# Kernel tuning notes

Measured on AMD Instinct MI355X. Metric: run time of the kernel, lower is better.

Reference implementation:

```python
import jax, jax.numpy as jnp
import numpy as np

HEADS = 12
DIM_HEAD = 64
SCALE = DIM_HEAD ** -0.5


def setup_inputs() -> dict:
    key = jax.random.key(0)
    ks = jax.random.split(key, 7)
    b, n, dim = 16, 1024, 768
    inner = HEADS * DIM_HEAD
    x = jax.random.normal(ks[0], (b, n, dim), dtype=jnp.float32)
    Wq = jax.random.normal(ks[1], (dim, inner), dtype=jnp.float32) * (dim ** -0.5)
    Wkv = jax.random.normal(ks[2], (dim, 2 * inner), dtype=jnp.float32) * (dim ** -0.5)
    mix_pre = jax.random.normal(ks[3], (HEADS, HEADS), dtype=jnp.float32)
    mix_post = jax.random.normal(ks[4], (HEADS, HEADS), dtype=jnp.float32)
    Wo = jax.random.normal(ks[5], (inner, dim), dtype=jnp.float32) * (inner ** -0.5)
    bo = jnp.zeros((dim,), dtype=jnp.float32)
    return {"x": x, "Wq": Wq, "Wkv": Wkv, "mix_pre": mix_pre,
            "mix_post": mix_post, "Wo": Wo, "bo": bo}


def reference(x, Wq, Wkv, mix_pre, mix_post, Wo, bo):
    b, n, dim = x.shape
    h, d = HEADS, DIM_HEAD
    # projections (context is None -> context = x)
    q = (x @ Wq).reshape(b, n, h, d).transpose(0, 2, 1, 3)        # b h n d
    kv = x @ Wkv
    k = kv[..., : h * d].reshape(b, n, h, d).transpose(0, 2, 1, 3)
    v = kv[..., h * d:].reshape(b, n, h, d).transpose(0, 2, 1, 3)
    # scaled QK^T
    attn = jnp.einsum('bhid,bhjd->bhij', q, k) * SCALE             # b h n n
    # talking-heads pre-softmax: mix over head dim
    attn = jnp.einsum('bhij,hg->bgij', attn, mix_pre)
    attn = jax.nn.softmax(attn, axis=-1)
    # talking-heads post-softmax
    attn = jnp.einsum('bhij,hg->bgij', attn, mix_post)
    out = jnp.einsum('bhij,bhjd->bhid', attn, v)                   # b h n d
    out = out.transpose(0, 2, 1, 3).reshape(b, n, h * d)           # b n (h d)
    return out @ Wo + bo
```

## Files before the change

kernel.cpp:

```cpp
#include <hip/hip_runtime.h>


typedef _Float16 f16;
typedef _Float16 f16x8 __attribute__((ext_vector_type(8)));
typedef _Float16 f16x4 __attribute__((ext_vector_type(4)));
typedef float f32x4 __attribute__((ext_vector_type(4)));
typedef float fv4 __attribute__((ext_vector_type(4)));

#define MFMA(a, b, c) __builtin_amdgcn_mfma_f32_16x16x32_f16(a, b, c, 0, 0, 0)
#define MFMA16(a, b, c) __builtin_amdgcn_mfma_f32_16x16x16f16(a, b, c, 0, 0, 0)

__global__ __launch_bounds__(256) void k_cast_x(const float* __restrict__ x,
                                                f16* __restrict__ xb) {
  int idx = (blockIdx.x * 256 + threadIdx.x) * 8;
  fv4 a = *(const fv4*)(x + idx);
  fv4 b = *(const fv4*)(x + idx + 4);
  f16x8 o;
  o[0] = (f16)a[0]; o[1] = (f16)a[1]; o[2] = (f16)a[2]; o[3] = (f16)a[3];
  o[4] = (f16)b[0]; o[5] = (f16)b[1]; o[6] = (f16)b[2]; o[7] = (f16)b[3];
  *(f16x8*)(xb + idx) = o;
}

__global__ __launch_bounds__(256) void k_prep_w(const float* __restrict__ Wq,
                                                const float* __restrict__ Wkv,
                                                const float* __restrict__ Wo,
                                                f16* __restrict__ Wt,
                                                f16* __restrict__ WoT) {
  int idx = blockIdx.x * 256 + threadIdx.x;
  if (idx < 2304 * 768) {
    int n = idx / 768, k = idx % 768;
    float v = (n < 768) ? Wq[k * 768 + n] * 0.125f
                        : Wkv[k * 1536 + (n - 768)];
    Wt[idx] = (f16)v;
  } else {
    int id2 = idx - 2304 * 768;
    int n = id2 / 768, k = id2 % 768;
    WoT[id2] = (f16)Wo[k * 768 + n];
  }
}

__global__ __launch_bounds__(256) void k_gemm_qkv(const f16* __restrict__ A,
                                                  const f16* __restrict__ Bt,
                                                  f16* __restrict__ qb,
                                                  f16* __restrict__ kb,
                                                  f16* __restrict__ vb) {
  __shared__ f16 As[128 * 72];
  __shared__ f16 Bs[128 * 72];
  const int tid = threadIdx.x;
  const int m0 = blockIdx.y << 7;
  const int n0 = blockIdx.x << 7;
  const int lane = tid & 63, w = tid >> 6;
  const int quad = lane >> 4, col = lane & 15;
  const int wm = (w >> 1) << 6, wn = (w & 1) << 6;
  const f32x4 z4 = {0.f, 0.f, 0.f, 0.f};
  f32x4 acc[4][4];
#pragma unroll
  for (int i = 0; i < 4; ++i)
#pragma unroll
    for (int j = 0; j < 4; ++j) acc[i][j] = z4;

  for (int k0 = 0; k0 < 768; k0 += 64) {
#pragma unroll
    for (int s = 0; s < 4; ++s) {
      int u = s * 256 + tid;
      int row = u >> 3, seg = (u & 7) << 3;
      *(f16x8*)&As[row * 72 + seg] = *(const f16x8*)(A + (m0 + row) * 768 + k0 + seg);
      *(f16x8*)&Bs[row * 72 + seg] = *(const f16x8*)(Bt + (n0 + row) * 768 + k0 + seg);
    }
    __syncthreads();
#pragma unroll
    for (int kk = 0; kk < 64; kk += 32) {
      f16x8 af[4], bf[4];
#pragma unroll
      for (int ic = 0; ic < 4; ++ic)
        af[ic] = *(f16x8*)&As[(wm + ic * 16 + col) * 72 + kk + quad * 8];
#pragma unroll
      for (int jc = 0; jc < 4; ++jc)
        bf[jc] = *(f16x8*)&Bs[(wn + jc * 16 + col) * 72 + kk + quad * 8];
#pragma unroll
      for (int ic = 0; ic < 4; ++ic)
#pragma unroll
        for (int jc = 0; jc < 4; ++jc) acc[ic][jc] = MFMA(af[ic], bf[jc], acc[ic][jc]);
    }
    __syncthreads();
  }
#pragma unroll
  for (int jc = 0; jc < 4; ++jc) {
    int gn = n0 + wn + jc * 16 + col;
#pragma unroll
    for (int ic = 0; ic < 4; ++ic)
#pragma unroll
      for (int r = 0; r < 4; ++r) {
        int gm = m0 + wm + ic * 16 + (quad << 2) + r;
        int b = gm >> 10, i = gm & 1023;
        f16 v = (f16)acc[ic][jc][r];
        if (gn < 768) {
          int h = gn >> 6, dd = gn & 63;
          qb[(((b * 12 + h) << 10) + i) * 64 + dd] = v;
        } else if (gn < 1536) {
          int t = gn - 768; int h = t >> 6, dd = t & 63;
          kb[(((b * 12 + h) << 10) + i) * 64 + dd] = v;
        } else {
          int t = gn - 1536; int h = t >> 6, dd = t & 63;
          vb[(((b * 12 + h) << 10) + i) * 64 + dd] = v;
        }
      }
  }
}

__global__ __launch_bounds__(256) void k_transpose_v(const f16* __restrict__ vb,
                                                     f16* __restrict__ vt) {
  __shared__ f16 t[64 * 72];
  const int bh = blockIdx.x;
  const int n0 = blockIdx.y << 6;
  const int tid = threadIdx.x;
#pragma unroll
  for (int s = 0; s < 2; ++s) {
    int u = s * 256 + tid;
    int r = u >> 3, c = (u & 7) << 3;
    *(f16x8*)&t[r * 72 + c] = *(const f16x8*)(vb + (bh * 1024 + n0 + r) * 64 + c);
  }
  __syncthreads();
#pragma unroll
  for (int s = 0; s < 2; ++s) {
    int u = s * 256 + tid;
    int d = u >> 3, c = (u & 7) << 3;
    f16x8 o;
#pragma unroll
    for (int e = 0; e < 8; ++e) o[e] = t[(c + e) * 72 + d];
    *(f16x8*)(vt + (bh * 64 + d) * 1024 + n0 + c) = o;
  }
}

__global__ __launch_bounds__(256, 2) void k_attn(
    const f16* __restrict__ qb, const f16* __restrict__ kb, const f16* __restrict__ vt,
    const float* __restrict__ mixp, const float* __restrict__ mixq,
    f16* __restrict__ ob) {
  __shared__ f16 Slds[4][4096];
  __shared__ f16 Pmb[12 * 16 * 16 * 4];

  const int tid = threadIdx.x;
  const int bid0 = blockIdx.x;
  const int bid = ((bid0 & 7) << 7) | (bid0 >> 3);
  const int b = bid >> 6;
  const int i0 = (bid & 63) << 4;
  const int lane = tid & 63;
  const int w = tid >> 6;
  const int quad = lane >> 4, col = lane & 15;
  const int q4 = quad << 2;
  const int w3 = w * 3;
  const int jw = w << 4;
  const f32x4 z4 = {0.f, 0.f, 0.f, 0.f};

  f16x4 b_pre, b_post;
#pragma unroll
  for (int e = 0; e < 4; ++e) {
    int hk = q4 + e;
    bool ok = (hk < 12) && (col < 12);
    b_pre[e]  = ok ? (f16)mixp[hk * 12 + col] : (f16)0.f;
    b_post[e] = ok ? (f16)mixq[hk * 12 + col] : (f16)0.f;
  }

  f16* Sw = &Slds[w][0];
  {
    f16x4 z; z[0] = (f16)0.f; z[1] = (f16)0.f; z[2] = (f16)0.f; z[3] = (f16)0.f;
#pragma unroll
    for (int u = 0; u < 4; ++u) {
      int idx = u * 64 + lane;
      *(f16x4*)&Sw[(((idx >> 4) << 6) + 48 + (idx & 15)) * 4] = z;
    }
  }

  f16x8 qf[12][2];
#pragma unroll
  for (int h = 0; h < 12; ++h)
#pragma unroll
    for (int kc = 0; kc < 2; ++kc)
      qf[h][kc] = *(const f16x8*)(qb + ((((b * 12 + h) << 10) + i0 + col) << 6) +
                                  kc * 32 + quad * 8);

  auto stage = [&](int j0) {
#pragma unroll
    for (int hg = 0; hg < 3; ++hg) {
      f32x4 s4[4];
#pragma unroll
      for (int e = 0; e < 4; ++e) {
        int h = hg * 4 + e;
        const f16* kbase = kb + ((((b * 12 + h) << 10) + j0 + jw + col) << 6);
        f16x8 kf0 = *(const f16x8*)(kbase + quad * 8);
        f16x8 kf1 = *(const f16x8*)(kbase + 32 + quad * 8);
        f32x4 a = MFMA(qf[h][0], kf0, z4);
        s4[e] = MFMA(qf[h][1], kf1, a);
      }
#pragma unroll
      for (int r = 0; r < 4; ++r) {
        f16x4 p;
        p[0] = (f16)s4[0][r]; p[1] = (f16)s4[1][r];
        p[2] = (f16)s4[2][r]; p[3] = (f16)s4[3][r];
        *(f16x4*)&Sw[((col << 6) + hg * 16 + ((q4 + r + col) & 15)) * 4] = p;
      }
    }
  };

  float l_run[4] = {0.f, 0.f, 0.f, 0.f};
  for (int j0 = 0; j0 < 1024; j0 += 64) {
    stage(j0);
#pragma unroll
    for (int t = 0; t < 16; ++t) {
      f16x4 sB = *(const f16x4*)&Sw[((t << 6) + quad * 16 + ((col + t) & 15)) * 4];
      f32x4 d1 = MFMA16(b_pre, sB, z4);
#pragma unroll
      for (int r = 0; r < 4; ++r) l_run[r] += __expf(d1[r]);
    }
  }
  float* Lb = (float*)Pmb;
#pragma unroll
  for (int r = 0; r < 4; ++r) Lb[(w * 16 + q4 + r) * 16 + col] = l_run[r];
  __syncthreads();
  float il[4];
#pragma unroll
  for (int r = 0; r < 4; ++r) {
    float s = 0.f;
#pragma unroll
    for (int ww = 0; ww < 4; ++ww) s += Lb[(ww * 16 + q4 + r) * 16 + col];
    il[r] = 1.f / s;
  }
  __syncthreads();

  f32x4 oa[3][4];
#pragma unroll
  for (int g = 0; g < 3; ++g)
#pragma unroll
    for (int dc = 0; dc < 4; ++dc) oa[g][dc] = z4;

  for (int j0 = 0; j0 < 1024; j0 += 64) {
    stage(j0);
#pragma unroll
    for (int tt = 0; tt < 4; ++tt) {
      f16x4 pk[4];
#pragma unroll
      for (int t4 = 0; t4 < 4; ++t4) {
        int t = tt * 4 + t4;
        f16x4 sB = *(const f16x4*)&Sw[((t << 6) + quad * 16 + ((col + t) & 15)) * 4];
        f32x4 d1 = MFMA16(b_pre, sB, z4);
        f16x4 pA;
#pragma unroll
        for (int r = 0; r < 4; ++r) pA[r] = (f16)(__expf(d1[r]) * il[r]);
        f32x4 d2 = MFMA16(pA, b_post, z4);
#pragma unroll
        for (int r = 0; r < 4; ++r) pk[r][t4] = (f16)d2[r];
      }
      if (col < 12) {
#pragma unroll
        for (int r = 0; r < 4; ++r) {
          int k4 = (col + q4 + r) & 15;
          *(f16x4*)&Pmb[(((col << 4) + q4 + r) * 16 + ((w * 4 + tt) ^ k4)) * 4] = pk[r];
        }
      }
    }
    __syncthreads();
    __builtin_amdgcn_s_setprio(1);
#pragma unroll
    for (int gg = 0; gg < 3; ++gg) {
      int gp = w3 + gg;
      int k4r = (gp + col) & 15;
#pragma unroll
      for (int jh = 0; jh < 2; ++jh) {
        int ub = (jh * 4 + quad) * 2;
        f16x4 lo = *(const f16x4*)&Pmb[(((gp << 4) + col) * 16 + (ub ^ k4r)) * 4];
        f16x4 hi = *(const f16x4*)&Pmb[(((gp << 4) + col) * 16 + ((ub + 1) ^ k4r)) * 4];
        f16x8 aP = __builtin_shufflevector(lo, hi, 0, 1, 2, 3, 4, 5, 6, 7);
#pragma unroll
        for (int dc = 0; dc < 4; ++dc) {
          f16x8 vf = *(const f16x8*)(vt + ((((b * 12 + gp) << 6) + dc * 16 + col) << 10) +
                                     j0 + jh * 32 + quad * 8);
          oa[gg][dc] = MFMA(aP, vf, oa[gg][dc]);
        }
      }
    }
    __builtin_amdgcn_s_setprio(0);
    __syncthreads();
  }

#pragma unroll
  for (int gg = 0; gg < 3; ++gg) {
    int gp = w3 + gg;
#pragma unroll
    for (int dc = 0; dc < 4; ++dc)
#pragma unroll
      for (int r = 0; r < 4; ++r)
        ob[((b << 10) + i0 + q4 + r) * 768 + gp * 64 + dc * 16 + col] =
            (f16)oa[gg][dc][r];
  }
}

__global__ __launch_bounds__(256) void k_gemm_out(const f16* __restrict__ A,
                                                  const f16* __restrict__ Bt,
                                                  const float* __restrict__ bias,
                                                  float* __restrict__ out) {
  __shared__ f16 As[128 * 72];
  __shared__ f16 Bs[128 * 72];
  const int tid = threadIdx.x;
  const int m0 = blockIdx.y << 7;
  const int n0 = blockIdx.x << 7;
  const int lane = tid & 63, w = tid >> 6;
  const int quad = lane >> 4, col = lane & 15;
  const int wm = (w >> 1) << 6, wn = (w & 1) << 6;
  const f32x4 z4 = {0.f, 0.f, 0.f, 0.f};
  f32x4 acc[4][4];
#pragma unroll
  for (int i = 0; i < 4; ++i)
#pragma unroll
    for (int j = 0; j < 4; ++j) acc[i][j] = z4;

  for (int k0 = 0; k0 < 768; k0 += 64) {
#pragma unroll
    for (int s = 0; s < 4; ++s) {
      int u = s * 256 + tid;
      int row = u >> 3, seg = (u & 7) << 3;
      *(f16x8*)&As[row * 72 + seg] = *(const f16x8*)(A + (m0 + row) * 768 + k0 + seg);
      *(f16x8*)&Bs[row * 72 + seg] = *(const f16x8*)(Bt + (n0 + row) * 768 + k0 + seg);
    }
    __syncthreads();
#pragma unroll
    for (int kk = 0; kk < 64; kk += 32) {
      f16x8 af[4], bf[4];
#pragma unroll
      for (int ic = 0; ic < 4; ++ic)
        af[ic] = *(f16x8*)&As[(wm + ic * 16 + col) * 72 + kk + quad * 8];
#pragma unroll
      for (int jc = 0; jc < 4; ++jc)
        bf[jc] = *(f16x8*)&Bs[(wn + jc * 16 + col) * 72 + kk + quad * 8];
#pragma unroll
      for (int ic = 0; ic < 4; ++ic)
#pragma unroll
        for (int jc = 0; jc < 4; ++jc) acc[ic][jc] = MFMA(af[ic], bf[jc], acc[ic][jc]);
    }
    __syncthreads();
  }
#pragma unroll
  for (int jc = 0; jc < 4; ++jc) {
    int gn = n0 + wn + jc * 16 + col;
    float bv = bias[gn];
#pragma unroll
    for (int ic = 0; ic < 4; ++ic)
#pragma unroll
      for (int r = 0; r < 4; ++r) {
        int gm = m0 + wm + ic * 16 + (quad << 2) + r;
        out[gm * 768 + gn] = acc[ic][jc][r] + bv;
      }
  }
}

extern "C" void kernel_launch(void* const* d_in, const int* in_sizes, int n_in,
                              void* d_out, int out_size, void* d_ws, size_t ws_size,
                              hipStream_t stream) {
  const float* x    = (const float*)d_in[0];
  const float* Wq   = (const float*)d_in[1];
  const float* Wkv  = (const float*)d_in[2];
  const float* mixp = (const float*)d_in[3];
  const float* mixq = (const float*)d_in[4];
  const float* Wo   = (const float*)d_in[5];
  const float* bo   = (const float*)d_in[6];
  float* out = (float*)d_out;

  char* ws = (char*)d_ws;
  f16* xb  = (f16*)(ws);
  f16* Wt  = (f16*)(ws + 25165824);
  f16* WoT = (f16*)(ws + 28704768);
  f16* qb  = (f16*)(ws + 29884416);
  f16* kb  = (f16*)(ws + 55050240);
  f16* vb  = (f16*)(ws + 80216064);
  f16* vt  = xb;
  f16* obuf = vb;

  k_cast_x<<<dim3(6144), dim3(256), 0, stream>>>(x, xb);
  k_prep_w<<<dim3(9216), dim3(256), 0, stream>>>(Wq, Wkv, Wo, Wt, WoT);
  k_gemm_qkv<<<dim3(18, 128), dim3(256), 0, stream>>>(xb, Wt, qb, kb, vb);
  k_transpose_v<<<dim3(192, 16), dim3(256), 0, stream>>>(vb, vt);
  k_attn<<<dim3(1024), dim3(256), 0, stream>>>(qb, kb, vt, mixp, mixq, obuf);
  k_gemm_out<<<dim3(6, 128), dim3(256), 0, stream>>>(obuf, WoT, bo, out);
}
```

Baseline: 827.8 us.

## Process 32 query rows per attention block with 8 waves

Each attention block now covers 32 query rows with 512 threads (8 waves) instead of 16 rows with 4 waves. Two wave groups split the rows and share the P-matrix exchange, so each block's V loads serve twice as many query rows. Shared memory becomes dynamic and grows to 112 KB per block, which limits how many blocks fit per CU and can lower occupancy.

```diff
diff --git a/kernel.cpp b/kernel.cpp
--- a/kernel.cpp
+++ b/kernel.cpp
@@ -132,24 +132,26 @@
   }
 }
 
-__global__ __launch_bounds__(256, 2) void k_attn(
+__global__ __launch_bounds__(512, 2) void k_attn(
     const f16* __restrict__ qb, const f16* __restrict__ kb, const f16* __restrict__ vt,
     const float* __restrict__ mixp, const float* __restrict__ mixq,
     f16* __restrict__ ob) {
-  __shared__ f16 Slds[4][4096];
-  __shared__ f16 Pmb[12 * 16 * 16 * 4];
+  extern __shared__ f16 smem[];
+  f16* Slds = smem;
+  f16* Pmb  = smem + 8 * 4096;
 
   const int tid = threadIdx.x;
   const int bid0 = blockIdx.x;
-  const int bid = ((bid0 & 7) << 7) | (bid0 >> 3);
-  const int b = bid >> 6;
-  const int i0 = (bid & 63) << 4;
+  const int bid = ((bid0 & 7) << 6) | (bid0 >> 3);
+  const int b = bid >> 5;
+  const int i0 = (bid & 31) << 5;
   const int lane = tid & 63;
   const int w = tid >> 6;
   const int quad = lane >> 4, col = lane & 15;
   const int q4 = quad << 2;
-  const int w3 = w * 3;
-  const int jw = w << 4;
+  const int ih = w >> 2;
+  const int jq = w & 3;
+  const int jw = jq << 4;
   const f32x4 z4 = {0.f, 0.f, 0.f, 0.f};
 
   f16x4 b_pre, b_post;
@@ -161,7 +163,7 @@
     b_post[e] = ok ? (f16)mixq[hk * 12 + col] : (f16)0.f;
   }
 
-  f16* Sw = &Slds[w][0];
+  f16* Sw = &Slds[w * 4096];
   {
     f16x4 z; z[0] = (f16)0.f; z[1] = (f16)0.f; z[2] = (f16)0.f; z[3] = (f16)0.f;
 #pragma unroll
@@ -176,7 +178,7 @@
   for (int h = 0; h < 12; ++h)
 #pragma unroll
     for (int kc = 0; kc < 2; ++kc)
-      qf[h][kc] = *(const f16x8*)(qb + ((((b * 12 + h) << 10) + i0 + col) << 6) +
+      qf[h][kc] = *(const f16x8*)(qb + ((((b * 12 + h) << 10) + i0 + ih * 16 + col) << 6) +
                                   kc * 32 + quad * 8);
 
   auto stage = [&](int j0) {
@@ -215,14 +217,14 @@
   }
   float* Lb = (float*)Pmb;
 #pragma unroll
-  for (int r = 0; r < 4; ++r) Lb[(w * 16 + q4 + r) * 16 + col] = l_run[r];
+  for (int r = 0; r < 4; ++r) Lb[w * 256 + (q4 + r) * 16 + col] = l_run[r];
   __syncthreads();
   float il[4];
 #pragma unroll
   for (int r = 0; r < 4; ++r) {
     float s = 0.f;
 #pragma unroll
-    for (int ww = 0; ww < 4; ++ww) s += Lb[(ww * 16 + q4 + r) * 16 + col];
+    for (int jj = 0; jj < 4; ++jj) s += Lb[(ih * 4 + jj) * 256 + (q4 + r) * 16 + col];
     il[r] = 1.f / s;
   }
   __syncthreads();
@@ -253,8 +255,9 @@
       if (col < 12) {
 #pragma unroll
         for (int r = 0; r < 4; ++r) {
-          int k4 = (col + q4 + r) & 15;
-          *(f16x4*)&Pmb[(((col << 4) + q4 + r) * 16 + ((w * 4 + tt) ^ k4)) * 4] = pk[r];
+          int iL = ih * 16 + q4 + r;
+          int k4 = (col + iL) & 15;
+          *(f16x4*)&Pmb[((col * 32 + iL) * 16 + (((jq << 2) + tt) ^ k4)) * 4] = pk[r];
         }
       }
     }
@@ -262,13 +265,15 @@
     __builtin_amdgcn_s_setprio(1);
 #pragma unroll
     for (int gg = 0; gg < 3; ++gg) {
-      int gp = w3 + gg;
-      int k4r = (gp + col) & 15;
+      int id = w * 3 + gg;
+      int gp = id >> 1, ihp = id & 1;
+      int row = gp * 32 + ihp * 16 + col;
+      int k4r = (gp + ihp * 16 + col) & 15;
 #pragma unroll
       for (int jh = 0; jh < 2; ++jh) {
         int ub = (jh * 4 + quad) * 2;
-        f16x4 lo = *(const f16x4*)&Pmb[(((gp << 4) + col) * 16 + (ub ^ k4r)) * 4];
-        f16x4 hi = *(const f16x4*)&Pmb[(((gp << 4) + col) * 16 + ((ub + 1) ^ k4r)) * 4];
+        f16x4 lo = *(const f16x4*)&Pmb[(row * 16 + (ub ^ k4r)) * 4];
+        f16x4 hi = *(const f16x4*)&Pmb[(row * 16 + ((ub + 1) ^ k4r)) * 4];
         f16x8 aP = __builtin_shufflevector(lo, hi, 0, 1, 2, 3, 4, 5, 6, 7);
 #pragma unroll
         for (int dc = 0; dc < 4; ++dc) {
@@ -284,12 +289,13 @@
 
 #pragma unroll
   for (int gg = 0; gg < 3; ++gg) {
-    int gp = w3 + gg;
+    int id = w * 3 + gg;
+    int gp = id >> 1, ihp = id & 1;
 #pragma unroll
     for (int dc = 0; dc < 4; ++dc)
 #pragma unroll
       for (int r = 0; r < 4; ++r)
-        ob[((b << 10) + i0 + q4 + r) * 768 + gp * 64 + dc * 16 + col] =
+        ob[((b << 10) + i0 + ihp * 16 + q4 + r) * 768 + gp * 64 + dc * 16 + col] =
             (f16)oa[gg][dc][r];
   }
 }
@@ -378,6 +384,6 @@
   k_prep_w<<<dim3(9216), dim3(256), 0, stream>>>(Wq, Wkv, Wo, Wt, WoT);
   k_gemm_qkv<<<dim3(18, 128), dim3(256), 0, stream>>>(xb, Wt, qb, kb, vb);
   k_transpose_v<<<dim3(192, 16), dim3(256), 0, stream>>>(vb, vt);
-  k_attn<<<dim3(1024), dim3(256), 0, stream>>>(qb, kb, vt, mixp, mixq, obuf);
+  k_attn<<<dim3(512), dim3(512), 114688, stream>>>(qb, kb, vt, mixp, mixq, obuf);
   k_gemm_out<<<dim3(6, 128), dim3(256), 0, stream>>>(obuf, WoT, bo, out);
 }
```

Measured after the change: 872.7 us. 1.05x slower.

## Stage Q tile in swizzled LDS instead of registers and compact score buffer

Applied to the files above, without the earlier changes.

The per-thread Q fragments (24 f16x8 registers) are moved into a swizzled shared-memory tile that is reloaded inside each QK^T stage, with the aim of cutting VGPR pressure in the attention kernel. The per-wave score buffer is compacted from 4096 to 3200 halves, so the unused fourth head group now reads a single shared zero row. Shared memory moves to a dynamic allocation of about 73 KB per block. In exchange, every stage issues extra LDS reads, and the larger LDS footprint may itself cap occupancy below the two blocks per CU the launch bounds target.

```diff
diff --git a/kernel.cpp b/kernel.cpp
--- a/kernel.cpp
+++ b/kernel.cpp
@@ -136,8 +136,10 @@
     const f16* __restrict__ qb, const f16* __restrict__ kb, const f16* __restrict__ vt,
     const float* __restrict__ mixp, const float* __restrict__ mixq,
     f16* __restrict__ ob) {
-  __shared__ f16 Slds[4][4096];
-  __shared__ f16 Pmb[12 * 16 * 16 * 4];
+  extern __shared__ f16 smem[];
+  f16* Qs   = smem;
+  f16* Slds = smem + 12288;
+  f16* Pmb  = smem + 25088;
 
   const int tid = threadIdx.x;
   const int bid0 = blockIdx.x;
@@ -161,23 +163,20 @@
     b_post[e] = ok ? (f16)mixq[hk * 12 + col] : (f16)0.f;
   }
 
-  f16* Sw = &Slds[w][0];
-  {
+  f16* Sw = &Slds[w * 3200];
+  if (lane < 16) {
     f16x4 z; z[0] = (f16)0.f; z[1] = (f16)0.f; z[2] = (f16)0.f; z[3] = (f16)0.f;
-#pragma unroll
-    for (int u = 0; u < 4; ++u) {
-      int idx = u * 64 + lane;
-      *(f16x4*)&Sw[(((idx >> 4) << 6) + 48 + (idx & 15)) * 4] = z;
-    }
-  }
-
-  f16x8 qf[12][2];
-#pragma unroll
-  for (int h = 0; h < 12; ++h)
-#pragma unroll
-    for (int kc = 0; kc < 2; ++kc)
-      qf[h][kc] = *(const f16x8*)(qb + ((((b * 12 + h) << 10) + i0 + col) << 6) +
-                                  kc * 32 + quad * 8);
+    *(f16x4*)&Sw[3072 + lane * 4] = z;
+  }
+
+#pragma unroll
+  for (int s = 0; s < 6; ++s) {
+    int u = s * 256 + tid;
+    int h = u >> 7, i = (u >> 3) & 15, uu = u & 7;
+    f16x8 q = *(const f16x8*)(qb + ((((b * 12 + h) << 10) + i0 + i) << 6) + uu * 8);
+    *(f16x8*)&Qs[(((h << 4) + i) << 6) + ((uu ^ (i & 7)) << 3)] = q;
+  }
+  __syncthreads();
 
   auto stage = [&](int j0) {
 #pragma unroll
@@ -189,17 +188,26 @@
         const f16* kbase = kb + ((((b * 12 + h) << 10) + j0 + jw + col) << 6);
         f16x8 kf0 = *(const f16x8*)(kbase + quad * 8);
         f16x8 kf1 = *(const f16x8*)(kbase + 32 + quad * 8);
-        f32x4 a = MFMA(qf[h][0], kf0, z4);
-        s4[e] = MFMA(qf[h][1], kf1, a);
+        f16x8 q0 = *(const f16x8*)&Qs[(((h << 4) + col) << 6) +
+                                      ((quad ^ (col & 7)) << 3)];
+        f16x8 q1 = *(const f16x8*)&Qs[(((h << 4) + col) << 6) +
+                                      (((4 + quad) ^ (col & 7)) << 3)];
+        f32x4 a = MFMA(q0, kf0, z4);
+        s4[e] = MFMA(q1, kf1, a);
       }
 #pragma unroll
       for (int r = 0; r < 4; ++r) {
         f16x4 p;
         p[0] = (f16)s4[0][r]; p[1] = (f16)s4[1][r];
         p[2] = (f16)s4[2][r]; p[3] = (f16)s4[3][r];
-        *(f16x4*)&Sw[((col << 6) + hg * 16 + ((q4 + r + col) & 15)) * 4] = p;
-      }
-    }
+        *(f16x4*)&Sw[col * 192 + hg * 64 + ((q4 + r + col) & 15) * 4] = p;
+      }
+    }
+  };
+  auto sread = [&](int t) -> f16x4 {
+    int zi = (quad < 3) ? (t * 192 + quad * 64 + ((col + t) & 15) * 4)
+                        : (3072 + ((col + t) & 15) * 4);
+    return *(const f16x4*)&Sw[zi];
   };
 
   float l_run[4] = {0.f, 0.f, 0.f, 0.f};
@@ -207,7 +215,7 @@
     stage(j0);
 #pragma unroll
     for (int t = 0; t < 16; ++t) {
-      f16x4 sB = *(const f16x4*)&Sw[((t << 6) + quad * 16 + ((col + t) & 15)) * 4];
+      f16x4 sB = sread(t);
       f32x4 d1 = MFMA16(b_pre, sB, z4);
 #pragma unroll
       for (int r = 0; r < 4; ++r) l_run[r] += __expf(d1[r]);
@@ -241,7 +249,7 @@
 #pragma unroll
       for (int t4 = 0; t4 < 4; ++t4) {
         int t = tt * 4 + t4;
-        f16x4 sB = *(const f16x4*)&Sw[((t << 6) + quad * 16 + ((col + t) & 15)) * 4];
+        f16x4 sB = sread(t);
         f32x4 d1 = MFMA16(b_pre, sB, z4);
         f16x4 pA;
 #pragma unroll
@@ -378,6 +386,6 @@
   k_prep_w<<<dim3(9216), dim3(256), 0, stream>>>(Wq, Wkv, Wo, Wt, WoT);
   k_gemm_qkv<<<dim3(18, 128), dim3(256), 0, stream>>>(xb, Wt, qb, kb, vb);
   k_transpose_v<<<dim3(192, 16), dim3(256), 0, stream>>>(vb, vt);
-  k_attn<<<dim3(1024), dim3(256), 0, stream>>>(qb, kb, vt, mixp, mixq, obuf);
+  k_attn<<<dim3(1024), dim3(256), 74752, stream>>>(qb, kb, vt, mixp, mixq, obuf);
   k_gemm_out<<<dim3(6, 128), dim3(256), 0, stream>>>(obuf, WoT, bo, out);
 }
```

New measurement: 770.3 us. -6.9%, faster.

## Restructure attention kernel to 8 waves with head/column split and double-buffered LDS

Applied to the files above, without the earlier changes.

The attention kernel now runs 8 waves per block instead of 4. Each wave owns 3 heads and one 16-column half of a 32-wide key chunk, replacing the 12-head-per-wave staging, so each wave holds fewer Q fragments in registers. S and P tiles are double-buffered in dynamic shared memory, V fragments are prefetched before the barrier, and blocks are remapped so each XCD handles whole batches. The aim is to cut register pressure and raise occupancy and latency hiding, at the cost of extra block-wide syncs per chunk and more LDS per block.

```diff
diff --git a/kernel.cpp b/kernel.cpp
--- a/kernel.cpp
+++ b/kernel.cpp
@@ -132,88 +132,85 @@
   }
 }
 
-__global__ __launch_bounds__(256, 2) void k_attn(
+__global__ __launch_bounds__(512, 4) void k_attn(
     const f16* __restrict__ qb, const f16* __restrict__ kb, const f16* __restrict__ vt,
     const float* __restrict__ mixp, const float* __restrict__ mixq,
     f16* __restrict__ ob) {
-  __shared__ f16 Slds[4][4096];
-  __shared__ f16 Pmb[12 * 16 * 16 * 4];
+  extern __shared__ f16 smem[];
 
   const int tid = threadIdx.x;
   const int bid0 = blockIdx.x;
-  const int bid = ((bid0 & 7) << 7) | (bid0 >> 3);
-  const int b = bid >> 6;
-  const int i0 = (bid & 63) << 4;
+  const int xcd = bid0 & 7, idx = bid0 >> 3;
+  const int b = ((idx >> 6) << 3) | xcd;
+  const int i0 = (idx & 63) << 4;
   const int lane = tid & 63;
   const int w = tid >> 6;
   const int quad = lane >> 4, col = lane & 15;
   const int q4 = quad << 2;
-  const int w3 = w * 3;
-  const int jw = w << 4;
+  const int hh = w >> 1;
+  const int jh = w & 1;
   const f32x4 z4 = {0.f, 0.f, 0.f, 0.f};
 
   f16x4 b_pre, b_post;
 #pragma unroll
   for (int e = 0; e < 4; ++e) {
+    b_pre[e]  = (e < 3 && col < 12) ? (f16)mixp[(3 * quad + e) * 12 + col] : (f16)0.f;
     int hk = q4 + e;
-    bool ok = (hk < 12) && (col < 12);
-    b_pre[e]  = ok ? (f16)mixp[hk * 12 + col] : (f16)0.f;
-    b_post[e] = ok ? (f16)mixq[hk * 12 + col] : (f16)0.f;
-  }
-
-  f16* Sw = &Slds[w][0];
-  {
-    f16x4 z; z[0] = (f16)0.f; z[1] = (f16)0.f; z[2] = (f16)0.f; z[3] = (f16)0.f;
-#pragma unroll
-    for (int u = 0; u < 4; ++u) {
-      int idx = u * 64 + lane;
-      *(f16x4*)&Sw[(((idx >> 4) << 6) + 48 + (idx & 15)) * 4] = z;
-    }
-  }
-
-  f16x8 qf[12][2];
-#pragma unroll
-  for (int h = 0; h < 12; ++h)
+    b_post[e] = (hk < 12 && col < 12) ? (f16)mixq[hk * 12 + col] : (f16)0.f;
+  }
+
+  f16x8 qf[3][2];
+#pragma unroll
+  for (int e = 0; e < 3; ++e)
 #pragma unroll
     for (int kc = 0; kc < 2; ++kc)
-      qf[h][kc] = *(const f16x8*)(qb + ((((b * 12 + h) << 10) + i0 + col) << 6) +
+      qf[e][kc] = *(const f16x8*)(qb + ((((b * 12 + 3 * hh + e) << 10) + i0 + col) << 6) +
                                   kc * 32 + quad * 8);
 
-  auto stage = [&](int j0) {
-#pragma unroll
-    for (int hg = 0; hg < 3; ++hg) {
-      f32x4 s4[4];
-#pragma unroll
-      for (int e = 0; e < 4; ++e) {
-        int h = hg * 4 + e;
-        const f16* kbase = kb + ((((b * 12 + h) << 10) + j0 + jw + col) << 6);
-        f16x8 kf0 = *(const f16x8*)(kbase + quad * 8);
-        f16x8 kf1 = *(const f16x8*)(kbase + 32 + quad * 8);
-        f32x4 a = MFMA(qf[h][0], kf0, z4);
-        s4[e] = MFMA(qf[h][1], kf1, a);
-      }
-#pragma unroll
-      for (int r = 0; r < 4; ++r) {
-        f16x4 p;
-        p[0] = (f16)s4[0][r]; p[1] = (f16)s4[1][r];
-        p[2] = (f16)s4[2][r]; p[3] = (f16)s4[3][r];
-        *(f16x4*)&Sw[((col << 6) + hg * 16 + ((q4 + r + col) & 15)) * 4] = p;
-      }
+  auto computeS = [&](int j0, f16* Sw) {
+    f16x8 kr[3][2];
+#pragma unroll
+    for (int e = 0; e < 3; ++e) {
+      const f16* kbase =
+          kb + ((((b * 12 + 3 * hh + e) << 10) + j0 + jh * 16 + col) << 6);
+      kr[e][0] = *(const f16x8*)(kbase + quad * 8);
+      kr[e][1] = *(const f16x8*)(kbase + 32 + quad * 8);
+    }
+    f32x4 s4[3];
+#pragma unroll
+    for (int e = 0; e < 3; ++e) {
+      f32x4 a = MFMA(qf[e][0], kr[e][0], z4);
+      s4[e] = MFMA(qf[e][1], kr[e][1], a);
+    }
+    int jj = jh * 16 + col;
+#pragma unroll
+    for (int r = 0; r < 4; ++r) {
+      f16x4 p;
+      p[0] = (f16)s4[0][r]; p[1] = (f16)s4[1][r]; p[2] = (f16)s4[2][r];
+      p[3] = (f16)0.f;
+      *(f16x4*)&Sw[((jj * 4 + hh) * 16 + ((q4 + r + col) & 15)) * 4] = p;
     }
   };
+  auto sread = [&](int t, const f16* Sw) -> f16x4 {
+    return *(const f16x4*)&Sw[((t * 4 + quad) * 16 + ((col + t) & 15)) * 4];
+  };
 
   float l_run[4] = {0.f, 0.f, 0.f, 0.f};
-  for (int j0 = 0; j0 < 1024; j0 += 64) {
-    stage(j0);
-#pragma unroll
-    for (int t = 0; t < 16; ++t) {
-      f16x4 sB = *(const f16x4*)&Sw[((t << 6) + quad * 16 + ((col + t) & 15)) * 4];
-      f32x4 d1 = MFMA16(b_pre, sB, z4);
+  for (int n = 0; n < 32; ++n) {
+    f16* Sw = smem + (n & 1) * 8192;
+    computeS(n * 32, Sw);
+    __syncthreads();
+    f16x4 sB[4];
+#pragma unroll
+    for (int t4 = 0; t4 < 4; ++t4) sB[t4] = sread(w * 4 + t4, Sw);
+#pragma unroll
+    for (int t4 = 0; t4 < 4; ++t4) {
+      f32x4 d1 = MFMA16(b_pre, sB[t4], z4);
 #pragma unroll
       for (int r = 0; r < 4; ++r) l_run[r] += __expf(d1[r]);
     }
   }
-  float* Lb = (float*)Pmb;
+  float* Lb = (float*)(smem + 16384);
 #pragma unroll
   for (int r = 0; r < 4; ++r) Lb[(w * 16 + q4 + r) * 16 + col] = l_run[r];
   __syncthreads();
@@ -222,75 +219,74 @@
   for (int r = 0; r < 4; ++r) {
     float s = 0.f;
 #pragma unroll
-    for (int ww = 0; ww < 4; ++ww) s += Lb[(ww * 16 + q4 + r) * 16 + col];
+    for (int ww = 0; ww < 8; ++ww) s += Lb[(ww * 16 + q4 + r) * 16 + col];
     il[r] = 1.f / s;
   }
   __syncthreads();
 
-  f32x4 oa[3][4];
-#pragma unroll
-  for (int g = 0; g < 3; ++g)
-#pragma unroll
-    for (int dc = 0; dc < 4; ++dc) oa[g][dc] = z4;
-
-  for (int j0 = 0; j0 < 1024; j0 += 64) {
-    stage(j0);
-#pragma unroll
-    for (int tt = 0; tt < 4; ++tt) {
-      f16x4 pk[4];
-#pragma unroll
-      for (int t4 = 0; t4 < 4; ++t4) {
-        int t = tt * 4 + t4;
-        f16x4 sB = *(const f16x4*)&Sw[((t << 6) + quad * 16 + ((col + t) & 15)) * 4];
-        f32x4 d1 = MFMA16(b_pre, sB, z4);
-        f16x4 pA;
-#pragma unroll
-        for (int r = 0; r < 4; ++r) pA[r] = (f16)(__expf(d1[r]) * il[r]);
-        f32x4 d2 = MFMA16(pA, b_post, z4);
-#pragma unroll
-        for (int r = 0; r < 4; ++r) pk[r][t4] = (f16)d2[r];
+  f32x4 oa[3][2];
+#pragma unroll
+  for (int u3 = 0; u3 < 3; ++u3) { oa[u3][0] = z4; oa[u3][1] = z4; }
+
+  for (int n = 0; n < 32; ++n) {
+    int j0 = n * 32;
+    f16* Sw = smem + (n & 1) * 8192;
+    f16* Pm = smem + 16384 + (n & 1) * 6144;
+    computeS(j0, Sw);
+    f16x8 vr[3][2];
+#pragma unroll
+    for (int u3 = 0; u3 < 3; ++u3) {
+      int u = w * 3 + u3, gp = u >> 1, dh = u & 1;
+#pragma unroll
+      for (int dc = 0; dc < 2; ++dc)
+        vr[u3][dc] = *(const f16x8*)(vt +
+            ((((b * 12 + gp) << 6) + dh * 32 + dc * 16 + col) << 10) + j0 + quad * 8);
+    }
+    __syncthreads();
+    f16x4 sB[4];
+#pragma unroll
+    for (int t4 = 0; t4 < 4; ++t4) sB[t4] = sread(w * 4 + t4, Sw);
+    f16x4 pk[4];
+#pragma unroll
+    for (int t4 = 0; t4 < 4; ++t4) {
+      f32x4 d1 = MFMA16(b_pre, sB[t4], z4);
+      f16x4 pA;
+#pragma unroll
+      for (int r = 0; r < 4; ++r) pA[r] = (f16)(__expf(d1[r]) * il[r]);
+      f32x4 d2 = MFMA16(pA, b_post, z4);
+#pragma unroll
+      for (int r = 0; r < 4; ++r) pk[r][t4] = (f16)d2[r];
+    }
+    if (col < 12) {
+#pragma unroll
+      for (int r = 0; r < 4; ++r) {
+        int k4 = (col + q4 + r) & 7;
+        *(f16x4*)&Pm[(((col << 4) + q4 + r) * 8 + (w ^ k4)) * 4] = pk[r];
       }
-      if (col < 12) {
-#pragma unroll
-        for (int r = 0; r < 4; ++r) {
-          int k4 = (col + q4 + r) & 15;
-          *(f16x4*)&Pmb[(((col << 4) + q4 + r) * 16 + ((w * 4 + tt) ^ k4)) * 4] = pk[r];
-        }
-      }
-    }
-    __syncthreads();
-    __builtin_amdgcn_s_setprio(1);
-#pragma unroll
-    for (int gg = 0; gg < 3; ++gg) {
-      int gp = w3 + gg;
-      int k4r = (gp + col) & 15;
-#pragma unroll
-      for (int jh = 0; jh < 2; ++jh) {
-        int ub = (jh * 4 + quad) * 2;
-        f16x4 lo = *(const f16x4*)&Pmb[(((gp << 4) + col) * 16 + (ub ^ k4r)) * 4];
-        f16x4 hi = *(const f16x4*)&Pmb[(((gp << 4) + col) * 16 + ((ub + 1) ^ k4r)) * 4];
-        f16x8 aP = __builtin_shufflevector(lo, hi, 0, 1, 2, 3, 4, 5, 6, 7);
-#pragma unroll
-        for (int dc = 0; dc < 4; ++dc) {
-          f16x8 vf = *(const f16x8*)(vt + ((((b * 12 + gp) << 6) + dc * 16 + col) << 10) +
-                                     j0 + jh * 32 + quad * 8);
-          oa[gg][dc] = MFMA(aP, vf, oa[gg][dc]);
-        }
-      }
-    }
-    __builtin_amdgcn_s_setprio(0);
-    __syncthreads();
-  }
-
-#pragma unroll
-  for (int gg = 0; gg < 3; ++gg) {
-    int gp = w3 + gg;
-#pragma unroll
-    for (int dc = 0; dc < 4; ++dc)
+    }
+    __syncthreads();
+#pragma unroll
+    for (int u3 = 0; u3 < 3; ++u3) {
+      int u = w * 3 + u3, gp = u >> 1;
+      int k4r = (gp + col) & 7;
+      f16x4 lo = *(const f16x4*)&Pm[(((gp << 4) + col) * 8 + ((quad * 2) ^ k4r)) * 4];
+      f16x4 hi = *(const f16x4*)&Pm[(((gp << 4) + col) * 8 + ((quad * 2 + 1) ^ k4r)) * 4];
+      f16x8 aP = __builtin_shufflevector(lo, hi, 0, 1, 2, 3, 4, 5, 6, 7);
+#pragma unroll
+      for (int dc = 0; dc < 2; ++dc)
+        oa[u3][dc] = MFMA(aP, vr[u3][dc], oa[u3][dc]);
+    }
+  }
+
+#pragma unroll
+  for (int u3 = 0; u3 < 3; ++u3) {
+    int u = w * 3 + u3, gp = u >> 1, dh = u & 1;
+#pragma unroll
+    for (int dc = 0; dc < 2; ++dc)
 #pragma unroll
       for (int r = 0; r < 4; ++r)
-        ob[((b << 10) + i0 + q4 + r) * 768 + gp * 64 + dc * 16 + col] =
-            (f16)oa[gg][dc][r];
+        ob[((b << 10) + i0 + q4 + r) * 768 + gp * 64 + dh * 32 + dc * 16 + col] =
+            (f16)oa[u3][dc][r];
   }
 }
 
@@ -378,6 +374,6 @@
   k_prep_w<<<dim3(9216), dim3(256), 0, stream>>>(Wq, Wkv, Wo, Wt, WoT);
   k_gemm_qkv<<<dim3(18, 128), dim3(256), 0, stream>>>(xb, Wt, qb, kb, vb);
   k_transpose_v<<<dim3(192, 16), dim3(256), 0, stream>>>(vb, vt);
-  k_attn<<<dim3(1024), dim3(256), 0, stream>>>(qb, kb, vt, mixp, mixq, obuf);
+  k_attn<<<dim3(1024), dim3(512), 57344, stream>>>(qb, kb, vt, mixp, mixq, obuf);
   k_gemm_out<<<dim3(6, 128), dim3(256), 0, stream>>>(obuf, WoT, bo, out);
 }
```

Measured after the change: 812.1 us. Within noise of the previous version (-1.9%).
